# Optimization experiments

Measured on AMD Instinct MI355X. Metric: run time of the kernel, lower is better.

Reference implementation:

```python
import jax, jax.numpy as jnp
import numpy as np

N_NODES = 50000
N_EDGES = 800000
IN_DIM = 256     # state_size
HID = 256        # hidden_dim
ACT = 64         # action_size


def gcn_conv(x, src, dst, norm, W, b):
    # PyG GCNConv: out[dst] += norm_e * (x @ W)[src]; then + bias
    h = x @ W                               # [N, out]
    msg = h[src] * norm[:, None]            # [E+N, out]
    agg = jax.ops.segment_sum(msg, dst, num_segments=N_NODES)
    return agg + b


def gcn_norm(edge_index):
    # add self-loops, symmetric normalization deg^-1/2[src]*deg^-1/2[dst]
    loops = jnp.arange(N_NODES, dtype=edge_index.dtype)
    src = jnp.concatenate([edge_index[0], loops])
    dst = jnp.concatenate([edge_index[1], loops])
    deg = jax.ops.segment_sum(jnp.ones_like(dst, dtype=jnp.float32), dst,
                              num_segments=N_NODES)
    dinv = jnp.where(deg > 0, jax.lax.rsqrt(deg), 0.0)
    norm = dinv[src] * dinv[dst]            # [E+N]
    return src, dst, norm


def setup_inputs() -> dict:
    key = jax.random.key(0)
    ks = jax.random.split(key, 12)
    x = jax.random.normal(ks[0], (N_NODES, IN_DIM), dtype=jnp.float32)
    edge_index = jax.random.randint(ks[1], (2, N_EDGES), 0, N_NODES, dtype=jnp.int64)

    def glorot(k, shape):
        lim = float(np.sqrt(6.0 / (shape[0] + shape[1])))
        return jax.random.uniform(k, shape, jnp.float32, -lim, lim)

    return {
        "x": x, "edge_index": edge_index,
        "W1": glorot(ks[2], (IN_DIM, HID)), "b1": jnp.zeros((HID,), jnp.float32),
        "W2": glorot(ks[3], (HID, HID)),    "b2": jnp.zeros((HID,), jnp.float32),
        "fcW1": glorot(ks[4], (HID, HID)),  "fcb1": jnp.zeros((HID,), jnp.float32),
        "fcW2": glorot(ks[5], (HID, HID)),  "fcb2": jnp.zeros((HID,), jnp.float32),
        "fcW3": glorot(ks[6], (HID, ACT)),  "fcb3": jnp.zeros((ACT,), jnp.float32),
    }


def reference(x, edge_index, W1, b1, W2, b2, fcW1, fcb1, fcW2, fcb2, fcW3, fcb3):
    src, dst, norm = gcn_norm(edge_index)
    h = jax.nn.relu(gcn_conv(x, src, dst, norm, W1, b1))   # GNNLayer 1
    h = jax.nn.relu(gcn_conv(h, src, dst, norm, W2, b2))   # GNNLayer 2
    g = jax.nn.relu(jnp.mean(h, axis=0)[None, :])          # [1, HID]
    g = jax.nn.relu(g @ fcW1 + fcb1)
    g = jax.nn.relu(g @ fcW2 + fcb2)
    return g @ fcW3 + fcb3                                 # [1, ACT]
```

## Files before the change

kernel.cpp:

```cpp
#include <hip/hip_runtime.h>

#define N_NODES 50000
#define N_EDGES 800000
#define DIM 256
#define ACT 64
#define SCAN_B 256
#define SCAN_NB ((N_NODES + SCAN_B - 1) / SCAN_B)
#define SLICE_ELEMS ((size_t)N_NODES * 32)
#define AGG_CHUNKS 512
#define TOTAL_GROUPS (AGG_CHUNKS * 32)
#define CSR_MAX (N_EDGES + 16 * N_NODES + 64)
#define NBINS 16
#define NBB (NBINS * SCAN_NB)

typedef __attribute__((ext_vector_type(8))) short short8_t;
typedef __attribute__((ext_vector_type(4))) float f32x4;
typedef __attribute__((ext_vector_type(4))) unsigned short ushort4_t;

__device__ __forceinline__ unsigned short f2b(float x) {
    unsigned u = __float_as_uint(x);
    unsigned r = u + 0x7FFFu + ((u >> 16) & 1u);
    return (unsigned short)(r >> 16);
}

__device__ __forceinline__ int deg_bin(int deg) {
    int rounds = ((deg + 16) & ~15) >> 4;
    return (rounds > NBINS - 1) ? NBINS - 1 : rounds;
}


__global__ __launch_bounds__(256) void k_cvt_wt2(const float* __restrict__ W1,
                                                 const float* __restrict__ W2,
                                                 unsigned short* __restrict__ W1t,
                                                 unsigned short* __restrict__ W2t) {
    int b = blockIdx.x;
    const float* W = (b < 256) ? W1 : W2;
    unsigned short* Wt = (b < 256) ? W1t : W2t;
    int i = (b & 255) * 256 + threadIdx.x;
    int k = i >> 8, n = i & 255;
    Wt[n * DIM + k] = f2b(W[k * DIM + n]);
}


__global__ void k_deg_count(const int* __restrict__ ei, int* degi) {
    int e = blockIdx.x * blockDim.x + threadIdx.x;
    if (e < N_EDGES) atomicAdd(&degi[ei[N_EDGES + e]], 1);
}


__global__ __launch_bounds__(256) void k_hist_rank(const int* __restrict__ degi,
                                                   int* blockbin,
                                                   unsigned char* lrank) {
    __shared__ int lh[NBINS];
    int t = threadIdx.x;
    if (t < NBINS) lh[t] = 0;
    __syncthreads();
    int i = blockIdx.x * 256 + t;
    if (i < N_NODES) {
        int bin = deg_bin(degi[i]);
        lrank[i] = (unsigned char)atomicAdd(&lh[bin], 1);
    }
    __syncthreads();
    if (t < NBINS) blockbin[t * SCAN_NB + blockIdx.x] = lh[t];
}

__global__ __launch_bounds__(256) void k_scan_bins(const int* __restrict__ blockbin,
                                                   int* blockbase) {
    __shared__ int sm[256];
    int t = threadIdx.x;
    const int CH = (NBB + 255) / 256;
    int s0 = t * CH;
    int s1 = s0 + CH; if (s1 > NBB) s1 = NBB;
    int s = 0;
    for (int i = s0; i < s1; ++i) s += blockbin[i];
    sm[t] = s;
    __syncthreads();
#pragma unroll
    for (int off = 1; off < 256; off <<= 1) {
        int u = (t >= off) ? sm[t - off] : 0;
        __syncthreads();
        sm[t] += u;
        __syncthreads();
    }
    int base = sm[t] - s;
    for (int i = s0; i < s1; ++i) { int v = blockbin[i]; blockbase[i] = base; base += v; }
}

__global__ __launch_bounds__(256) void k_perm_apply(const int* __restrict__ degi,
                                                    const int* __restrict__ blockbase,
                                                    const unsigned char* __restrict__ lrank,
                                                    int* perm) {
    int i = blockIdx.x * 256 + threadIdx.x;
    if (i >= N_NODES) return;
    int bin = deg_bin(degi[i]);
    perm[blockbase[bin * SCAN_NB + blockIdx.x] + lrank[i]] = i;
}


__global__ __launch_bounds__(SCAN_B) void k_scan_local(const int* __restrict__ degi,
                                                       const int* __restrict__ perm,
                                                       int* lexc, int* btot) {
    __shared__ int sm[SCAN_B];
    int t = threadIdx.x;
    int i = blockIdx.x * SCAN_B + t;
    int v = (i < N_NODES) ? ((degi[perm[i]] + 16) & ~15) : 0;
    sm[t] = v;
    __syncthreads();
#pragma unroll
    for (int off = 1; off < SCAN_B; off <<= 1) {
        int u = (t >= off) ? sm[t - off] : 0;
        __syncthreads();
        sm[t] += u;
        __syncthreads();
    }
    if (i < N_NODES) lexc[i] = sm[t] - v;
    if (t == SCAN_B - 1) btot[blockIdx.x] = sm[t];
}

__global__ __launch_bounds__(SCAN_B) void k_scan_tops(const int* __restrict__ btot,
                                                      int* bbase, int* rowstart) {
    __shared__ int sm[SCAN_B];
    int t = threadIdx.x;
    int v = (t < SCAN_NB) ? btot[t] : 0;
    sm[t] = v;
    __syncthreads();
#pragma unroll
    for (int off = 1; off < SCAN_B; off <<= 1) {
        int u = (t >= off) ? sm[t - off] : 0;
        __syncthreads();
        sm[t] += u;
        __syncthreads();
    }
    if (t < SCAN_NB) bbase[t] = sm[t] - v;
    if (t == SCAN_NB - 1) rowstart[N_NODES] = sm[t];
}

__global__ __launch_bounds__(SCAN_B) void k_scan_apply(const int* __restrict__ degi,
                                                       const int* __restrict__ perm,
                                                       const int* __restrict__ lexc,
                                                       const int* __restrict__ bbase,
                                                       int* rowstart, int* fillpos,
                                                       float* dinv, unsigned* csr4) {
    int i = blockIdx.x * SCAN_B + threadIdx.x;
    if (i >= N_NODES) return;
    int rs = bbase[blockIdx.x] + lexc[i];
    rowstart[i] = rs;
    int n = perm[i];
    int d = degi[n] + 1;
    float di = rsqrtf((float)d);
    dinv[n] = di;
    csr4[rs] = ((unsigned)n << 16) | f2b(di * di);
    fillpos[n] = rs + 1;
}

__global__ void k_fill_edge(const int* __restrict__ ei,
                            const float* __restrict__ dinv, int* fillpos,
                            unsigned* csr4) {
    int e = blockIdx.x * blockDim.x + threadIdx.x;
    if (e < N_EDGES) {
        int s = ei[e];
        int d = ei[N_EDGES + e];
        int p = atomicAdd(&fillpos[d], 1);
        csr4[p] = ((unsigned)s << 16) | f2b(dinv[s] * dinv[d]);
    }
}


template <int AFP32>
__global__ __launch_bounds__(512) void k_gemm_mfma(const void* __restrict__ Ap,
                                                   const unsigned short* __restrict__ Wt,
                                                   unsigned short* __restrict__ H,
                                                   int M) {
    __shared__ char lds[49152];
    char* AsB = lds;
    char* BsB = lds + 16384;

    int tid = threadIdx.x;
    int w = tid >> 6;
    int l = tid & 63;
    int wr = w >> 2, wc = w & 3;
    int r0 = blockIdx.x * 128;

    f32x4 acc[4][4];
#pragma unroll
    for (int i = 0; i < 4; ++i)
#pragma unroll
        for (int j = 0; j < 4; ++j) acc[i][j] = (f32x4)(0.f);

    for (int kt = 0; kt < 4; ++kt) {
        int k0 = kt * 64;
#pragma unroll
        for (int i = 0; i < 2; ++i) {
            int c = tid + i * 512;
            int row = c >> 3, kc = c & 7;
            int gg = r0 + row; if (gg >= M) gg = M - 1;
            short8_t v;
            if (AFP32) {
                const float* A = (const float*)Ap;
                const float4* src = (const float4*)(A + (size_t)gg * DIM + k0 + kc * 8);
                float4 f0 = src[0], f1 = src[1];
                v[0] = (short)f2b(f0.x); v[1] = (short)f2b(f0.y);
                v[2] = (short)f2b(f0.z); v[3] = (short)f2b(f0.w);
                v[4] = (short)f2b(f1.x); v[5] = (short)f2b(f1.y);
                v[6] = (short)f2b(f1.z); v[7] = (short)f2b(f1.w);
            } else {
                const unsigned short* A = (const unsigned short*)Ap;
                int k = k0 + kc * 8;
                int slice = k >> 5, within = k & 31;
                v = *(const short8_t*)(A + (size_t)slice * SLICE_ELEMS + (size_t)gg * 32 + within);
            }
            int off = (row * 128 + kc * 16) ^ ((row & 7) << 4);
            *(short8_t*)(AsB + off) = v;
        }
#pragma unroll
        for (int i = 0; i < 4; ++i) {
            int c = tid + i * 512;
            int n = c >> 3, kc = c & 7;
            short8_t v = *(const short8_t*)(Wt + n * DIM + k0 + kc * 8);
            int off = (n * 128 + kc * 16) ^ ((n & 7) << 4);
            *(short8_t*)(BsB + off) = v;
        }
        __syncthreads();

#pragma unroll
        for (int kf = 0; kf < 2; ++kf) {
            int kb = kf * 64 + (l >> 4) * 16;
            short8_t a[4], b[4];
#pragma unroll
            for (int fm = 0; fm < 4; ++fm) {
                int ra = wr * 64 + fm * 16 + (l & 15);
                a[fm] = *(const short8_t*)(AsB + ((ra * 128 + kb) ^ ((ra & 7) << 4)));
            }
#pragma unroll
            for (int fn = 0; fn < 4; ++fn) {
                int nb = wc * 64 + fn * 16 + (l & 15);
                b[fn] = *(const short8_t*)(BsB + ((nb * 128 + kb) ^ ((nb & 7) << 4)));
            }
#pragma unroll
            for (int fm = 0; fm < 4; ++fm)
#pragma unroll
                for (int fn = 0; fn < 4; ++fn)
                    acc[fm][fn] = __builtin_amdgcn_mfma_f32_16x16x32_bf16(
                        a[fm], b[fn], acc[fm][fn], 0, 0, 0);
        }
        __syncthreads();
    }

#pragma unroll
    for (int fm = 0; fm < 4; ++fm) {
#pragma unroll
        for (int i = 0; i < 4; ++i) {
            int row = r0 + wr * 64 + fm * 16 + ((l >> 4) << 2) + i;
            if (row >= M) continue;
#pragma unroll
            for (int fn = 0; fn < 4; ++fn) {
                int col = wc * 64 + fn * 16 + (l & 15);
                int slice = col >> 5;
                H[(size_t)slice * SLICE_ELEMS + (size_t)row * 32 + (col & 31)] = f2b(acc[fm][fn][i]);
            }
        }
    }
}


__global__ __launch_bounds__(256) void k_agg_sliced(const unsigned short* __restrict__ H,
                                                    const int* __restrict__ rowstart,
                                                    const unsigned* __restrict__ csr4,
                                                    const int* __restrict__ perm,
                                                    const float* __restrict__ bias,
                                                    unsigned short* __restrict__ X,
                                                    float* __restrict__ gsum,
                                                    int write_out) {
    __shared__ unsigned pbuf[32 * 68];
    int slice = blockIdx.x & 7;
    int chunk = blockIdx.x >> 3;
    int g = threadIdx.x >> 3;
    int lane = threadIdx.x & 7;
    const char* Hb = (const char*)(H + (size_t)slice * SLICE_ELEMS) + (lane << 3);
    unsigned short* Xs = X + (size_t)slice * SLICE_ELEMS;
    int d0 = slice * 32 + lane * 4;
    float4 bb = *(const float4*)&bias[d0];
    float c0 = 0.f, c1 = 0.f, c2 = 0.f, c3 = 0.f;
    unsigned* ps = pbuf + g * 68;
    int fg = chunk * 32 + g;
    for (int idx = fg; idx < N_NODES; idx += TOTAL_GROUPS) {
        int n = perm[idx];
        int beg = rowstart[idx], end = rowstart[idx + 1];
        float a0 = 0.f, a1 = 0.f, a2 = 0.f, a3 = 0.f;
        uint4 u = *(const uint4*)(csr4 + beg + (lane << 2));
        int r = 0;
        for (int e = beg; e < end; e += 32, ++r) {
            int en = (e + 32 < end) ? e + 32 : e;
            uint4 un = *(const uint4*)(csr4 + en + (lane << 2));
            unsigned* pb = ps + (r & 1) * 32;
            *(uint4*)(pb + (lane << 2)) = u;
#pragma unroll
            for (int s = 0; s < 2; ++s) {
                if (e + (s << 4) >= end) break;
                unsigned pp[16];
#pragma unroll
                for (int i = 0; i < 16; ++i) pp[i] = pb[(s << 4) + i];
                uint2 q[16];
#pragma unroll
                for (int i = 0; i < 16; ++i)
                    q[i] = *(const uint2*)(Hb + ((pp[i] >> 16) << 6));
#pragma unroll
                for (int i = 0; i < 16; ++i) {
                    float nm = __uint_as_float(pp[i] << 16);
                    a0 = fmaf(nm, __uint_as_float(q[i].x << 16), a0);
                    a1 = fmaf(nm, __uint_as_float(q[i].x & 0xFFFF0000u), a1);
                    a2 = fmaf(nm, __uint_as_float(q[i].y << 16), a2);
                    a3 = fmaf(nm, __uint_as_float(q[i].y & 0xFFFF0000u), a3);
                }
            }
            u = un;
        }
        float o0 = fmaxf(a0 + bb.x, 0.f);
        float o1 = fmaxf(a1 + bb.y, 0.f);
        float o2 = fmaxf(a2 + bb.z, 0.f);
        float o3 = fmaxf(a3 + bb.w, 0.f);
        if (write_out) {
            ushort4_t o; o.x = f2b(o0); o.y = f2b(o1); o.z = f2b(o2); o.w = f2b(o3);
            *(ushort4_t*)(Xs + (size_t)n * 32 + (lane << 2)) = o;
        }
        c0 += o0; c1 += o1; c2 += o2; c3 += o3;
    }
    if (gsum) {
        __shared__ float4 smr[256];
        int tid = threadIdx.x;
        smr[tid] = make_float4(c0, c1, c2, c3);
        __syncthreads();
#pragma unroll
        for (int off = 128; off >= 8; off >>= 1) {
            if (tid < off) {
                float4 a = smr[tid], b = smr[tid + off];
                smr[tid] = make_float4(a.x + b.x, a.y + b.y, a.z + b.z, a.w + b.w);
            }
            __syncthreads();
        }
        if (tid < 8) {
            float4 v = smr[tid];
            atomicAdd(&gsum[d0], v.x);
            atomicAdd(&gsum[d0 + 1], v.y);
            atomicAdd(&gsum[d0 + 2], v.z);
            atomicAdd(&gsum[d0 + 3], v.w);
        }
    }
}


__global__ __launch_bounds__(256) void k_fc(const float* __restrict__ gsum,
                                            const float* __restrict__ fcW1,
                                            const float* __restrict__ fcb1,
                                            const float* __restrict__ fcW2,
                                            const float* __restrict__ fcb2,
                                            const float* __restrict__ fcW3,
                                            const float* __restrict__ fcb3,
                                            float* __restrict__ out) {
    __shared__ float g[DIM];
    __shared__ float h[DIM];
    int t = threadIdx.x;
    g[t] = fmaxf(gsum[t] * (1.0f / (float)N_NODES), 0.f);
    __syncthreads();
    float acc = fcb1[t];
    for (int k = 0; k < DIM; ++k) acc = fmaf(g[k], fcW1[k * DIM + t], acc);
    h[t] = fmaxf(acc, 0.f);
    __syncthreads();
    acc = fcb2[t];
    for (int k = 0; k < DIM; ++k) acc = fmaf(h[k], fcW2[k * DIM + t], acc);
    __syncthreads();
    g[t] = fmaxf(acc, 0.f);
    __syncthreads();
    if (t < ACT) {
        float o = fcb3[t];
        for (int k = 0; k < DIM; ++k) o = fmaf(g[k], fcW3[k * ACT + t], o);
        out[t] = o;
    }
}


extern "C" void kernel_launch(void* const* d_in, const int* in_sizes, int n_in,
                              void* d_out, int out_size, void* d_ws, size_t ws_size,
                              hipStream_t stream) {
    const float* x    = (const float*)d_in[0];
    const int*   ei   = (const int*)d_in[1];
    const float* W1   = (const float*)d_in[2];
    const float* b1   = (const float*)d_in[3];
    const float* W2   = (const float*)d_in[4];
    const float* b2   = (const float*)d_in[5];
    const float* fcW1 = (const float*)d_in[6];
    const float* fcb1 = (const float*)d_in[7];
    const float* fcW2 = (const float*)d_in[8];
    const float* fcb2 = (const float*)d_in[9];
    const float* fcW3 = (const float*)d_in[10];
    const float* fcb3 = (const float*)d_in[11];
    float* out = (float*)d_out;

    char* w = (char*)d_ws;
    size_t o = 0;
#define CARVE(name, type, count) \
    type* name = (type*)(w + o); \
    o += (((size_t)(count) * sizeof(type)) + 255) & ~(size_t)255;
    CARVE(degi, int, N_NODES)
    CARVE(rowstart, int, N_NODES + 1)
    CARVE(fillpos, int, N_NODES)
    CARVE(dinv, float, N_NODES)
    CARVE(lexc, int, N_NODES)
    CARVE(btot, int, SCAN_NB)
    CARVE(bbase, int, SCAN_NB)
    CARVE(blockbin, int, NBB)
    CARVE(blockbase, int, NBB)
    CARVE(perm, int, N_NODES)
    CARVE(lrank, unsigned char, N_NODES)
    CARVE(csr4, unsigned, CSR_MAX)
    CARVE(gsum, float, DIM)
    CARVE(W1t, unsigned short, DIM * DIM)
    CARVE(W2t, unsigned short, DIM * DIM)
    CARVE(Hbuf, unsigned short, (size_t)N_NODES * DIM)
    CARVE(Xbuf, unsigned short, (size_t)N_NODES * DIM)
#undef CARVE

    hipMemsetAsync(gsum, 0, DIM * sizeof(float), stream);
    hipMemsetAsync(degi, 0, N_NODES * sizeof(int), stream);
    hipMemsetAsync(csr4, 0, (size_t)CSR_MAX * sizeof(unsigned), stream);

    k_cvt_wt2<<<512, 256, 0, stream>>>(W1, W2, W1t, W2t);

    k_deg_count<<<(N_EDGES + 255) / 256, 256, 0, stream>>>(ei, degi);
    k_hist_rank<<<SCAN_NB, 256, 0, stream>>>(degi, blockbin, lrank);
    k_scan_bins<<<1, 256, 0, stream>>>(blockbin, blockbase);
    k_perm_apply<<<SCAN_NB, 256, 0, stream>>>(degi, blockbase, lrank, perm);
    k_scan_local<<<SCAN_NB, SCAN_B, 0, stream>>>(degi, perm, lexc, btot);
    k_scan_tops<<<1, SCAN_B, 0, stream>>>(btot, bbase, rowstart);
    k_scan_apply<<<SCAN_NB, SCAN_B, 0, stream>>>(degi, perm, lexc, bbase, rowstart,
                                                 fillpos, dinv, csr4);
    k_fill_edge<<<(N_EDGES + 255) / 256, 256, 0, stream>>>(ei, dinv, fillpos, csr4);

    int gemm_grid = (N_NODES + 127) / 128;
    k_gemm_mfma<1><<<gemm_grid, 512, 0, stream>>>(x, W1t, Hbuf, N_NODES);
    k_agg_sliced<<<8 * AGG_CHUNKS, 256, 0, stream>>>(Hbuf, rowstart, csr4, perm, b1,
                                                     Xbuf, (float*)nullptr, 1);
    k_gemm_mfma<0><<<gemm_grid, 512, 0, stream>>>(Xbuf, W2t, Hbuf, N_NODES);
    k_agg_sliced<<<8 * AGG_CHUNKS, 256, 0, stream>>>(Hbuf, rowstart, csr4, perm, b2,
                                                     Xbuf, gsum, 0);

    k_fc<<<1, 256, 0, stream>>>(gsum, fcW1, fcb1, fcW2, fcb2, fcW3, fcb3, out);
}
```

Baseline: 281.4 us.

## Sort nodes by descending degree, split FC head into multi-block kernels, merge memsets

Reverses the degree-bin order so high-degree nodes are processed first in the aggregation, which should reduce tail imbalance. Replaces the single-block FC head with three small kernels that spread each matrix-vector product over 16 (or 4) blocks, with a split-K reduction in shared memory. Merges the gsum and degi memsets into one by placing the two buffers next to each other. The FC split adds two extra kernel launches in exchange for more parallelism.

```diff
diff --git a/kernel.cpp b/kernel.cpp
--- a/kernel.cpp
+++ b/kernel.cpp
@@ -23,9 +23,10 @@
     return (unsigned short)(r >> 16);
 }
 
-__device__ __forceinline__ int deg_bin(int deg) {
+__device__ __forceinline__ int deg_bin_desc(int deg) {
     int rounds = ((deg + 16) & ~15) >> 4;
-    return (rounds > NBINS - 1) ? NBINS - 1 : rounds;
+    if (rounds > NBINS - 1) rounds = NBINS - 1;
+    return (NBINS - 1) - rounds;
 }
 
 
@@ -57,7 +58,7 @@
     __syncthreads();
     int i = blockIdx.x * 256 + t;
     if (i < N_NODES) {
-        int bin = deg_bin(degi[i]);
+        int bin = deg_bin_desc(degi[i]);
         lrank[i] = (unsigned char)atomicAdd(&lh[bin], 1);
     }
     __syncthreads();
@@ -92,7 +93,7 @@
                                                     int* perm) {
     int i = blockIdx.x * 256 + threadIdx.x;
     if (i >= N_NODES) return;
-    int bin = deg_bin(degi[i]);
+    int bin = deg_bin_desc(degi[i]);
     perm[blockbase[bin * SCAN_NB + blockIdx.x] + lrank[i]] = i;
 }
 
@@ -349,32 +350,33 @@
 }
 
 
-__global__ __launch_bounds__(256) void k_fc(const float* __restrict__ gsum,
-                                            const float* __restrict__ fcW1,
-                                            const float* __restrict__ fcb1,
-                                            const float* __restrict__ fcW2,
-                                            const float* __restrict__ fcb2,
-                                            const float* __restrict__ fcW3,
-                                            const float* __restrict__ fcb3,
-                                            float* __restrict__ out) {
-    __shared__ float g[DIM];
-    __shared__ float h[DIM];
+template <int STRIDE, int RELU_IN, int RELU_OUT>
+__global__ __launch_bounds__(256) void k_fcx(const float* __restrict__ gin,
+                                             const float* __restrict__ W,
+                                             const float* __restrict__ bias,
+                                             float* __restrict__ gout,
+                                             float scale) {
+    __shared__ float red[16][17];
     int t = threadIdx.x;
-    g[t] = fmaxf(gsum[t] * (1.0f / (float)N_NODES), 0.f);
-    __syncthreads();
-    float acc = fcb1[t];
-    for (int k = 0; k < DIM; ++k) acc = fmaf(g[k], fcW1[k * DIM + t], acc);
-    h[t] = fmaxf(acc, 0.f);
-    __syncthreads();
-    acc = fcb2[t];
-    for (int k = 0; k < DIM; ++k) acc = fmaf(h[k], fcW2[k * DIM + t], acc);
-    __syncthreads();
-    g[t] = fmaxf(acc, 0.f);
-    __syncthreads();
-    if (t < ACT) {
-        float o = fcb3[t];
-        for (int k = 0; k < DIM; ++k) o = fmaf(g[k], fcW3[k * ACT + t], o);
-        out[t] = o;
+    int lo = t & 15;
+    int o = blockIdx.x * 16 + lo;
+    int kc = t >> 4;
+    float acc = 0.f;
+#pragma unroll
+    for (int i = 0; i < 16; ++i) {
+        int k = kc * 16 + i;
+        float gv = gin[k] * scale;
+        if (RELU_IN) gv = fmaxf(gv, 0.f);
+        acc = fmaf(gv, W[k * STRIDE + o], acc);
+    }
+    red[kc][lo] = acc;
+    __syncthreads();
+    if (t < 16) {
+        float s = bias[blockIdx.x * 16 + t];
+#pragma unroll
+        for (int j = 0; j < 16; ++j) s += red[j][t];
+        if (RELU_OUT) s = fmaxf(s, 0.f);
+        gout[blockIdx.x * 16 + t] = s;
     }
 }
 
@@ -402,6 +404,7 @@
     type* name = (type*)(w + o); \
     o += (((size_t)(count) * sizeof(type)) + 255) & ~(size_t)255;
     CARVE(degi, int, N_NODES)
+    CARVE(gsum, float, DIM)
     CARVE(rowstart, int, N_NODES + 1)
     CARVE(fillpos, int, N_NODES)
     CARVE(dinv, float, N_NODES)
@@ -413,15 +416,15 @@
     CARVE(perm, int, N_NODES)
     CARVE(lrank, unsigned char, N_NODES)
     CARVE(csr4, unsigned, CSR_MAX)
-    CARVE(gsum, float, DIM)
+    CARVE(g1, float, DIM)
+    CARVE(g2, float, DIM)
     CARVE(W1t, unsigned short, DIM * DIM)
     CARVE(W2t, unsigned short, DIM * DIM)
     CARVE(Hbuf, unsigned short, (size_t)N_NODES * DIM)
     CARVE(Xbuf, unsigned short, (size_t)N_NODES * DIM)
 #undef CARVE
 
-    hipMemsetAsync(gsum, 0, DIM * sizeof(float), stream);
-    hipMemsetAsync(degi, 0, N_NODES * sizeof(int), stream);
+    hipMemsetAsync(degi, 0, (size_t)((char*)rowstart - (char*)degi), stream);
     hipMemsetAsync(csr4, 0, (size_t)CSR_MAX * sizeof(unsigned), stream);
 
     k_cvt_wt2<<<512, 256, 0, stream>>>(W1, W2, W1t, W2t);
@@ -444,5 +447,7 @@
     k_agg_sliced<<<8 * AGG_CHUNKS, 256, 0, stream>>>(Hbuf, rowstart, csr4, perm, b2,
                                                      Xbuf, gsum, 0);
 
-    k_fc<<<1, 256, 0, stream>>>(gsum, fcW1, fcb1, fcW2, fcb2, fcW3, fcb3, out);
-}
+    k_fcx<DIM, 1, 1><<<16, 256, 0, stream>>>(gsum, fcW1, fcb1, g1, 1.0f / (float)N_NODES);
+    k_fcx<DIM, 0, 1><<<16, 256, 0, stream>>>(g1, fcW2, fcb2, g2, 1.0f);
+    k_fcx<ACT, 0, 0><<<4, 256, 0, stream>>>(g2, fcW3, fcb3, out, 1.0f);
+}
```

New measurement: 266.6 us. 5.3% less time.
